# Kernel optimization log

Hardware: AMD Instinct MI355X
Metric: run time of the kernel (lower is better)

Reference implementation:

```python
import jax, jax.numpy as jnp
import numpy as np

GROUP_SIZE = 256


def dequantize(qweight, scales, zeros, dtype):
    # qweight: [out, in] uint8-valued ints; scales/zeros: [n_groups, 1]
    out_f, in_f = qweight.shape
    w = qweight.astype(dtype).reshape(-1, GROUP_SIZE)
    w = (w - zeros) * scales
    return w.reshape(out_f, in_f)


def setup_inputs() -> dict:
    key = jax.random.key(0)
    k1, k2, k3, k4, k5 = jax.random.split(key, 5)
    B, S, IN, OUT = 4, 2048, 4096, 4096
    n_groups = OUT * IN // GROUP_SIZE
    x = jax.random.normal(k1, (B, S, IN), dtype=jnp.float32)
    qweight = jax.random.randint(k2, (OUT, IN), 0, 256, dtype=jnp.int32)
    scales = jax.random.uniform(k3, (n_groups, 1), dtype=jnp.float32) * 0.01 + 1e-4
    zeros = jax.random.randint(k4, (n_groups, 1), 0, 256).astype(jnp.float32)
    bias = jax.random.normal(k5, (OUT,), dtype=jnp.float32) * 0.02
    return {"x": x, "qweight": qweight, "scales": scales, "zeros": zeros, "bias": bias}


def reference(x, qweight, scales, zeros, bias):
    # float_weight = (qw - zeros) * scales, grouped along flattened weight
    w = dequantize(qweight, scales, zeros, x.dtype)  # [out, in]
    # y = x @ W^T + b
    return jnp.einsum("bsi,oi->bso", x, w) + bias
```

## Files before the change

### kernel.cpp

```cpp
#include <hip/hip_runtime.h>


typedef __attribute__((ext_vector_type(8))) short bf16x8;
typedef __attribute__((ext_vector_type(8))) unsigned short ushort8;
typedef __attribute__((ext_vector_type(4))) float f32x4;

__device__ inline unsigned short f2bf(float f) {
  union { float f; unsigned int u; } v; v.f = f;
  unsigned int u = v.u;
  return (unsigned short)((u + 0x7fffu + ((u >> 16) & 1u)) >> 16);
}

__global__ void prep_kernel(const int* __restrict__ q,
                            const float* __restrict__ sc,
                            const float* __restrict__ zp,
                            ushort8* __restrict__ wb,
                            const float* __restrict__ x,
                            ushort8* __restrict__ xb,
                            int nw8, int nx8) {
  int t = blockIdx.x * blockDim.x + threadIdx.x;
  if (t < nw8) {
    const int4* q4 = (const int4*)q + (size_t)t * 2;
    int4 a = q4[0];
    int4 b = q4[1];
    int g = t >> 5;
    float s = sc[g], z = zp[g];
    ushort8 o;
    o[0] = f2bf(((float)a.x - z) * s);
    o[1] = f2bf(((float)a.y - z) * s);
    o[2] = f2bf(((float)a.z - z) * s);
    o[3] = f2bf(((float)a.w - z) * s);
    o[4] = f2bf(((float)b.x - z) * s);
    o[5] = f2bf(((float)b.y - z) * s);
    o[6] = f2bf(((float)b.z - z) * s);
    o[7] = f2bf(((float)b.w - z) * s);
    wb[t] = o;
  } else {
    int u = t - nw8;
    if (u >= nx8) return;
    const float4* x4 = (const float4*)x + (size_t)u * 2;
    float4 a = x4[0];
    float4 b = x4[1];
    ushort8 o;
    o[0] = f2bf(a.x); o[1] = f2bf(a.y); o[2] = f2bf(a.z); o[3] = f2bf(a.w);
    o[4] = f2bf(b.x); o[5] = f2bf(b.y); o[6] = f2bf(b.z); o[7] = f2bf(b.w);
    xb[u] = o;
  }
}

#define BM 256
#define BN 256
#define BK 64

#define BAR() asm volatile("s_barrier" ::: "memory")
#define MFMA16(d, x, y) d = __builtin_amdgcn_mfma_f32_16x16x32_bf16(x, y, d, 0, 0, 0)

__device__ inline void gload_lds16(const void* g, void* l) {
  __builtin_amdgcn_global_load_lds(
      (const __attribute__((address_space(1))) unsigned int*)g,
      (__attribute__((address_space(3))) unsigned int*)l, 16, 0, 0);
}

__device__ inline void stage_half(const unsigned short* __restrict__ gsrc,
                                  char* lds_region, int K, int wave, int lane) {
  const int l3  = lane >> 3;
  const int swz = ((lane & 7) ^ l3) * 8;
#pragma unroll
  for (int inst = 0; inst < 2; ++inst) {
    const int row = inst * 64 + wave * 8 + l3;
    gload_lds16(gsrc + (size_t)row * K + swz,
                lds_region + (size_t)(inst * 512 + wave * 64) * 16);
  }
}

__global__ __launch_bounds__(512, 2)
void gemm256_kernel(const unsigned short* __restrict__ A,
                    const unsigned short* __restrict__ B,
                    const float* __restrict__ bias,
                    float* __restrict__ C,
                    int M, int N, int K) {
  extern __shared__ char lds[];
  const int t    = threadIdx.x;
  const int lane = t & 63;
  const int wave = t >> 6;
  const int wm   = wave >> 2;
  const int wn   = wave & 3;
  const int lr   = lane & 15;
  const int hi   = lane >> 4;
  const int l7   = lane & 7;

  const int nwg = gridDim.x;
  const int cpx = nwg >> 3;
  const int bid = blockIdx.x;
  const int swzb = (bid & 7) * cpx + (bid >> 3);
  const int ntn = N / BN;
  const int bm = swzb / ntn, bn = swzb % ntn;
  const int row0 = bm * BM, col0 = bn * BN;

  const int NT = K / BK;

  const int soff0 = ((hi) ^ l7) * 16;
  const int soff1 = ((4 + hi) ^ l7) * 16;

  const unsigned short* Asrc = A + (size_t)row0 * K;
  const unsigned short* Bsrc = B + (size_t)col0 * K;

#define STAGE_A0(buf, kt) stage_half(Asrc + (size_t)(kt) * BK,           (buf),         K, wave, lane)
#define STAGE_A1(buf, kt) stage_half(Asrc + (size_t)128 * K + (kt) * BK, (buf) + 16384, K, wave, lane)
#define STAGE_B0(buf, kt) stage_half(Bsrc + (size_t)(kt) * BK,           (buf) + 32768, K, wave, lane)
#define STAGE_B1(buf, kt) stage_half(Bsrc + (size_t)128 * K + (kt) * BK, (buf) + 49152, K, wave, lane)

  f32x4 acc[8][4] = {};
  bf16x8 a[4][2];
  bf16x8 b[4][2];

#define READ_A(mh, bufp) {                                                    \
    const char* Ab_ = (const char*)(bufp) + wm * 16384 + (mh) * 8192;         \
    _Pragma("unroll")                                                         \
    for (int mm = 0; mm < 4; ++mm) {                                          \
      const int r_ = (mm * 16 + lr) * 128;                                    \
      a[mm][0] = *(const bf16x8*)(Ab_ + r_ + soff0);                          \
      a[mm][1] = *(const bf16x8*)(Ab_ + r_ + soff1);                          \
    } }
#define READ_B(nh, bufp) {                                                    \
    const char* Bb_ = (const char*)(bufp) + 32768 + wn * 8192;                \
    _Pragma("unroll")                                                         \
    for (int nn = 0; nn < 2; ++nn) {                                          \
      const int r_ = (((nh) * 2 + nn) * 16 + lr) * 128;                       \
      b[(nh) * 2 + nn][0] = *(const bf16x8*)(Bb_ + r_ + soff0);               \
      b[(nh) * 2 + nn][1] = *(const bf16x8*)(Bb_ + r_ + soff1);               \
    } }
#define MFMA_QUAD(mh, nh)                                                     \
    __builtin_amdgcn_s_setprio(1);                                            \
    _Pragma("unroll")                                                         \
    for (int mm = 0; mm < 4; ++mm)                                            \
      _Pragma("unroll")                                                       \
      for (int nn = 0; nn < 2; ++nn) {                                        \
        MFMA16(acc[(mh) * 4 + mm][(nh) * 2 + nn], a[mm][0], b[(nh) * 2 + nn][0]); \
        MFMA16(acc[(mh) * 4 + mm][(nh) * 2 + nn], a[mm][1], b[(nh) * 2 + nn][1]); \
      }                                                                       \
    __builtin_amdgcn_s_setprio(0);

#define KT_BODY(buf, nbuf, kt, GUARDED)                                       \
  {                                                                           \
                      \
    BAR();                                                                    \
    MFMA_QUAD(0, 0);                                                          \
    if (!(GUARDED) || (kt) + 1 < NT) STAGE_A1(nbuf, (kt) + 1);                \
    READ_B(1, buf);                                                           \
                     \
    BAR();                                                                    \
    MFMA_QUAD(0, 1);                                                          \
    if (!(GUARDED) || (kt) + 2 < NT) STAGE_B0(buf, (kt) + 2);                 \
    READ_A(1, buf);                                                           \
                          \
    BAR();                                                                    \
    MFMA_QUAD(1, 0);                                                          \
    if (!(GUARDED) || (kt) + 2 < NT) {                                        \
      STAGE_B1(buf, (kt) + 2);                                                \
      asm volatile("s_waitcnt vmcnt(4)" ::: "memory");                        \
    } else {                                                                  \
      asm volatile("s_waitcnt vmcnt(0)" ::: "memory");                        \
    }                                                                         \
       \
    BAR();                                                                    \
    MFMA_QUAD(1, 1);                                                          \
    if (!(GUARDED) || (kt) + 2 < NT) STAGE_A0(buf, (kt) + 2);                 \
    if (!(GUARDED) || (kt) + 1 < NT) {                                        \
      READ_A(0, nbuf);                                                        \
      READ_B(0, nbuf);                                                        \
    }                                                                         \
  }

  char* buf0 = lds;
  char* buf1 = lds + 65536;
  STAGE_A0(buf0, 0); STAGE_A1(buf0, 0); STAGE_B0(buf0, 0); STAGE_B1(buf0, 0);
  STAGE_A0(buf1, 1); STAGE_B0(buf1, 1); STAGE_B1(buf1, 1);
  asm volatile("s_waitcnt vmcnt(6)" ::: "memory");
  BAR();
  READ_A(0, buf0);
  READ_B(0, buf0);

  int kt = 0;
  for (; kt + 3 < NT; kt += 2) {
    KT_BODY(buf0, buf1, kt, 0);
    KT_BODY(buf1, buf0, kt + 1, 0);
  }
  for (; kt < NT; ++kt) {
    char* buf  = lds + ((kt & 1) << 16);
    char* nbuf = lds + (((kt & 1) ^ 1) << 16);
    KT_BODY(buf, nbuf, kt, 1);
  }

  BAR();
  {
    char* myl = lds + wave * 16384;
    const int gcol = col0 + wn * 64 + lr * 4;
    const float4 bv4 = *(const float4*)&bias[gcol];
#pragma unroll
    for (int mp = 0; mp < 4; ++mp) {
#pragma unroll
      for (int mm = 0; mm < 2; ++mm)
#pragma unroll
        for (int n = 0; n < 4; ++n)
#pragma unroll
          for (int j = 0; j < 4; ++j)
            *(float*)(myl + (mm * 16 + hi * 4 + j) * 272 + (n * 16 + lr) * 4)
                = acc[mp * 2 + mm][n][j];
#pragma unroll
      for (int r = 0; r < 8; ++r) {
        const int row = r * 4 + hi;
        float4 v = *(const float4*)(myl + row * 272 + lr * 16);
        v.x += bv4.x; v.y += bv4.y; v.z += bv4.z; v.w += bv4.w;
        const int grow = row0 + wm * 128 + mp * 32 + row;
        *(float4*)&C[(size_t)grow * N + gcol] = v;
      }
    }
  }
#undef STAGE_A0
#undef STAGE_A1
#undef STAGE_B0
#undef STAGE_B1
#undef READ_A
#undef READ_B
#undef MFMA_QUAD
#undef KT_BODY
}

extern "C" void kernel_launch(void* const* d_in, const int* in_sizes, int n_in,
                              void* d_out, int out_size, void* d_ws, size_t ws_size,
                              hipStream_t stream) {
  const float* x      = (const float*)d_in[0];
  const int*   qw     = (const int*)d_in[1];
  const float* scales = (const float*)d_in[2];
  const float* zeros  = (const float*)d_in[3];
  const float* bias   = (const float*)d_in[4];
  float* out = (float*)d_out;

  const int OUT = in_sizes[4];
  const int IN  = in_sizes[1] / OUT;
  const int M   = in_sizes[0] / IN;

  unsigned short* wb = (unsigned short*)d_ws;
  unsigned short* xb = wb + (size_t)OUT * IN;

  {
    int nw8 = OUT * IN / 8;
    int nx8 = (int)((size_t)M * IN / 8);
    int total = nw8 + nx8;
    prep_kernel<<<(total + 255) / 256, 256, 0, stream>>>(
        qw, scales, zeros, (ushort8*)wb, x, (ushort8*)xb, nw8, nx8);
  }
  {
    hipFuncSetAttribute((const void*)gemm256_kernel,
                        hipFuncAttributeMaxDynamicSharedMemorySize, 131072);
    dim3 grid((M / BM) * (OUT / BN));
    gemm256_kernel<<<grid, 512, 131072, stream>>>(xb, wb, bias, out, M, OUT, IN);
  }
}
```

Before: 263.6 us.

## Fuse fp32-to-bf16 activation conversion into GEMM A-tile staging

Removes the separate pass that converts x to bf16 in a workspace. The GEMM now loads fp32 activations into registers, converts them to bf16 and writes them into swizzled LDS. The pipeline waits are reworked to fit the register-staged A path beside the direct-to-LDS B loads. This drops a full write and re-read of the bf16 activation buffer, at the cost of twice the A global traffic per tile (fp32), extra VALU conversion work, more registers and extra lgkmcnt waits inside the main loop.

```diff
diff --git a/kernel.cpp b/kernel.cpp
--- a/kernel.cpp
+++ b/kernel.cpp
@@ -11,41 +11,27 @@
   return (unsigned short)((u + 0x7fffu + ((u >> 16) & 1u)) >> 16);
 }
 
-__global__ void prep_kernel(const int* __restrict__ q,
-                            const float* __restrict__ sc,
-                            const float* __restrict__ zp,
-                            ushort8* __restrict__ wb,
-                            const float* __restrict__ x,
-                            ushort8* __restrict__ xb,
-                            int nw8, int nx8) {
+__global__ void dequant_w_kernel(const int* __restrict__ q,
+                                 const float* __restrict__ sc,
+                                 const float* __restrict__ zp,
+                                 ushort8* __restrict__ wb, int total8) {
   int t = blockIdx.x * blockDim.x + threadIdx.x;
-  if (t < nw8) {
-    const int4* q4 = (const int4*)q + (size_t)t * 2;
-    int4 a = q4[0];
-    int4 b = q4[1];
-    int g = t >> 5;
-    float s = sc[g], z = zp[g];
-    ushort8 o;
-    o[0] = f2bf(((float)a.x - z) * s);
-    o[1] = f2bf(((float)a.y - z) * s);
-    o[2] = f2bf(((float)a.z - z) * s);
-    o[3] = f2bf(((float)a.w - z) * s);
-    o[4] = f2bf(((float)b.x - z) * s);
-    o[5] = f2bf(((float)b.y - z) * s);
-    o[6] = f2bf(((float)b.z - z) * s);
-    o[7] = f2bf(((float)b.w - z) * s);
-    wb[t] = o;
-  } else {
-    int u = t - nw8;
-    if (u >= nx8) return;
-    const float4* x4 = (const float4*)x + (size_t)u * 2;
-    float4 a = x4[0];
-    float4 b = x4[1];
-    ushort8 o;
-    o[0] = f2bf(a.x); o[1] = f2bf(a.y); o[2] = f2bf(a.z); o[3] = f2bf(a.w);
-    o[4] = f2bf(b.x); o[5] = f2bf(b.y); o[6] = f2bf(b.z); o[7] = f2bf(b.w);
-    xb[u] = o;
-  }
+  if (t >= total8) return;
+  const int4* q4 = (const int4*)q + (size_t)t * 2;
+  int4 a = q4[0];
+  int4 b = q4[1];
+  int g = t >> 5;
+  float s = sc[g], z = zp[g];
+  ushort8 o;
+  o[0] = f2bf(((float)a.x - z) * s);
+  o[1] = f2bf(((float)a.y - z) * s);
+  o[2] = f2bf(((float)a.z - z) * s);
+  o[3] = f2bf(((float)a.w - z) * s);
+  o[4] = f2bf(((float)b.x - z) * s);
+  o[5] = f2bf(((float)b.y - z) * s);
+  o[6] = f2bf(((float)b.z - z) * s);
+  o[7] = f2bf(((float)b.w - z) * s);
+  wb[t] = o;
 }
 
 #define BM 256
@@ -74,8 +60,8 @@
 }
 
 __global__ __launch_bounds__(512, 2)
-void gemm256_kernel(const unsigned short* __restrict__ A,
-                    const unsigned short* __restrict__ B,
+void gemm256_kernel(const float* __restrict__ X,
+                    const unsigned short* __restrict__ Bw,
                     const float* __restrict__ bias,
                     float* __restrict__ C,
                     int M, int N, int K) {
@@ -89,6 +75,13 @@
   const int hi   = lane >> 4;
   const int l7   = lane & 7;
 
+  const int arow  = t >> 2;
+  const int asl0  = (t & 3) * 2;
+  const int asl1  = asl0 + 1;
+  const int arow7 = arow & 7;
+  const int aoff0 = (asl0 ^ arow7) * 16;
+  const int aoff1 = (asl1 ^ arow7) * 16;
+
   const int nwg = gridDim.x;
   const int cpx = nwg >> 3;
   const int bid = blockIdx.x;
@@ -102,17 +95,34 @@
   const int soff0 = ((hi) ^ l7) * 16;
   const int soff1 = ((4 + hi) ^ l7) * 16;
 
-  const unsigned short* Asrc = A + (size_t)row0 * K;
-  const unsigned short* Bsrc = B + (size_t)col0 * K;
-
-#define STAGE_A0(buf, kt) stage_half(Asrc + (size_t)(kt) * BK,           (buf),         K, wave, lane)
-#define STAGE_A1(buf, kt) stage_half(Asrc + (size_t)128 * K + (kt) * BK, (buf) + 16384, K, wave, lane)
+  const float* Ax = X + (size_t)row0 * K;
+  const unsigned short* Bsrc = Bw + (size_t)col0 * K;
+
 #define STAGE_B0(buf, kt) stage_half(Bsrc + (size_t)(kt) * BK,           (buf) + 32768, K, wave, lane)
 #define STAGE_B1(buf, kt) stage_half(Bsrc + (size_t)128 * K + (kt) * BK, (buf) + 49152, K, wave, lane)
+
+#define A_ISSUE(va, vb, vc, vd, half, kt) {                                   \
+    const float* g_ = Ax + ((size_t)((half) * 128 + arow)) * K + (size_t)(kt) * BK; \
+    va = *(const float4*)(g_ + asl0 * 8);                                     \
+    vb = *(const float4*)(g_ + asl0 * 8 + 4);                                 \
+    vc = *(const float4*)(g_ + asl1 * 8);                                     \
+    vd = *(const float4*)(g_ + asl1 * 8 + 4);                                 \
+  }
+#define A_WRITE(va, vb, vc, vd, regionp) {                                    \
+    ushort8 o0, o1;                                                           \
+    o0[0] = f2bf(va.x); o0[1] = f2bf(va.y); o0[2] = f2bf(va.z); o0[3] = f2bf(va.w); \
+    o0[4] = f2bf(vb.x); o0[5] = f2bf(vb.y); o0[6] = f2bf(vb.z); o0[7] = f2bf(vb.w); \
+    o1[0] = f2bf(vc.x); o1[1] = f2bf(vc.y); o1[2] = f2bf(vc.z); o1[3] = f2bf(vc.w); \
+    o1[4] = f2bf(vd.x); o1[5] = f2bf(vd.y); o1[6] = f2bf(vd.z); o1[7] = f2bf(vd.w); \
+    *(ushort8*)((regionp) + arow * 128 + aoff0) = o0;                         \
+    *(ushort8*)((regionp) + arow * 128 + aoff1) = o1;                         \
+  }
 
   f32x4 acc[8][4] = {};
   bf16x8 a[4][2];
   bf16x8 b[4][2];
+  float4 al0, al1, al2, al3;
+  float4 bl0, bl1, bl2, bl3;
 
 #define READ_A(mh, bufp) {                                                    \
     const char* Ab_ = (const char*)(bufp) + wm * 16384 + (mh) * 8192;         \
@@ -143,29 +153,31 @@
 
 #define KT_BODY(buf, nbuf, kt, GUARDED)                                       \
   {                                                                           \
-                      \
+                          \
     BAR();                                                                    \
     MFMA_QUAD(0, 0);                                                          \
-    if (!(GUARDED) || (kt) + 1 < NT) STAGE_A1(nbuf, (kt) + 1);                \
+    if (!(GUARDED) || (kt) + 1 < NT) A_ISSUE(bl0, bl1, bl2, bl3, 1, (kt) + 1);\
     READ_B(1, buf);                                                           \
-                     \
+                                                              \
     BAR();                                                                    \
     MFMA_QUAD(0, 1);                                                          \
     if (!(GUARDED) || (kt) + 2 < NT) STAGE_B0(buf, (kt) + 2);                 \
+    if (!(GUARDED)) { asm volatile("s_waitcnt vmcnt(6)" ::: "memory"); }      \
+    else if ((kt) + 1 < NT) { asm volatile("s_waitcnt vmcnt(0)" ::: "memory"); } \
+    if (!(GUARDED) || (kt) + 1 < NT) A_WRITE(al0, al1, al2, al3, (nbuf));     \
     READ_A(1, buf);                                                           \
-                          \
+                                                                   \
     BAR();                                                                    \
     MFMA_QUAD(1, 0);                                                          \
-    if (!(GUARDED) || (kt) + 2 < NT) {                                        \
-      STAGE_B1(buf, (kt) + 2);                                                \
-      asm volatile("s_waitcnt vmcnt(4)" ::: "memory");                        \
-    } else {                                                                  \
-      asm volatile("s_waitcnt vmcnt(0)" ::: "memory");                        \
-    }                                                                         \
-       \
+    if (!(GUARDED) || (kt) + 2 < NT) STAGE_B1(buf, (kt) + 2);                 \
+    if (!(GUARDED)) { asm volatile("s_waitcnt vmcnt(4)" ::: "memory"); }      \
+    else { asm volatile("s_waitcnt vmcnt(0)" ::: "memory"); }                 \
+    if (!(GUARDED) || (kt) + 1 < NT) A_WRITE(bl0, bl1, bl2, bl3, (nbuf) + 16384); \
+    asm volatile("s_waitcnt lgkmcnt(0)" ::: "memory");                        \
+          \
     BAR();                                                                    \
     MFMA_QUAD(1, 1);                                                          \
-    if (!(GUARDED) || (kt) + 2 < NT) STAGE_A0(buf, (kt) + 2);                 \
+    if (!(GUARDED) || (kt) + 2 < NT) A_ISSUE(al0, al1, al2, al3, 0, (kt) + 2);\
     if (!(GUARDED) || (kt) + 1 < NT) {                                        \
       READ_A(0, nbuf);                                                        \
       READ_B(0, nbuf);                                                        \
@@ -174,9 +186,18 @@
 
   char* buf0 = lds;
   char* buf1 = lds + 65536;
-  STAGE_A0(buf0, 0); STAGE_A1(buf0, 0); STAGE_B0(buf0, 0); STAGE_B1(buf0, 0);
-  STAGE_A0(buf1, 1); STAGE_B0(buf1, 1); STAGE_B1(buf1, 1);
-  asm volatile("s_waitcnt vmcnt(6)" ::: "memory");
+  {
+    float4 p0, p1, p2, p3, r0, r1, r2, r3;
+    A_ISSUE(p0, p1, p2, p3, 0, 0);
+    A_ISSUE(r0, r1, r2, r3, 1, 0);
+    asm volatile("s_waitcnt vmcnt(0)" ::: "memory");
+    A_WRITE(p0, p1, p2, p3, buf0);
+    A_WRITE(r0, r1, r2, r3, buf0 + 16384);
+  }
+  STAGE_B0(buf0, 0); STAGE_B1(buf0, 0);
+  STAGE_B0(buf1, 1); STAGE_B1(buf1, 1);
+  A_ISSUE(al0, al1, al2, al3, 0, 1);
+  asm volatile("s_waitcnt vmcnt(8) lgkmcnt(0)" ::: "memory");
   BAR();
   READ_A(0, buf0);
   READ_B(0, buf0);
@@ -217,10 +238,10 @@
       }
     }
   }
-#undef STAGE_A0
-#undef STAGE_A1
 #undef STAGE_B0
 #undef STAGE_B1
+#undef A_ISSUE
+#undef A_WRITE
 #undef READ_A
 #undef READ_B
 #undef MFMA_QUAD
@@ -242,19 +263,16 @@
   const int M   = in_sizes[0] / IN;
 
   unsigned short* wb = (unsigned short*)d_ws;
-  unsigned short* xb = wb + (size_t)OUT * IN;
-
-  {
-    int nw8 = OUT * IN / 8;
-    int nx8 = (int)((size_t)M * IN / 8);
-    int total = nw8 + nx8;
-    prep_kernel<<<(total + 255) / 256, 256, 0, stream>>>(
-        qw, scales, zeros, (ushort8*)wb, x, (ushort8*)xb, nw8, nx8);
+
+  {
+    int total8 = OUT * IN / 8;
+    dequant_w_kernel<<<(total8 + 255) / 256, 256, 0, stream>>>(
+        qw, scales, zeros, (ushort8*)wb, total8);
   }
   {
     hipFuncSetAttribute((const void*)gemm256_kernel,
                         hipFuncAttributeMaxDynamicSharedMemorySize, 131072);
     dim3 grid((M / BM) * (OUT / BN));
-    gemm256_kernel<<<grid, 512, 131072, stream>>>(xb, wb, bias, out, M, OUT, IN);
-  }
-}
+    gemm256_kernel<<<grid, 512, 131072, stream>>>(x, wb, bias, out, M, OUT, IN);
+  }
+}
```

Result: slower. 717.7 us (+172.2%).
